# Optimization experiments

Hardware: AMD Instinct MI355X
Metric: run time of the kernel (lower is better)

## Reference

```python
import jax, jax.numpy as jnp
import numpy as np


def setup_inputs() -> dict:
    key = jax.random.key(0)
    k_in, k_idx, k_neg, k_w, k_b = jax.random.split(key, 5)
    N, C_in, C_out, K, L = 8, 128, 256, 7, 16384
    x = jax.random.normal(k_in, (N, C_in, L), dtype=jnp.float32)
    idx = jax.random.randint(k_idx, (K, L), 0, L, dtype=jnp.int64)
    drop = jax.random.uniform(k_neg, (K, L)) < 0.05
    idx = jnp.where(drop, -1, idx)
    stdv = 1.0 / np.sqrt(C_in * K)
    weight = jax.random.uniform(k_w, (C_out, C_in, K), dtype=jnp.float32, minval=-stdv, maxval=stdv)
    bias = jax.random.uniform(k_b, (C_out,), dtype=jnp.float32, minval=-stdv, maxval=stdv)
    return {"input": x, "indices": idx, "weight": weight, "bias": bias}


def reference(input, indices, weight, bias):
    # indices: (K, L); -1 means zero-padding (matches utils.prepare_mask)
    mask = (indices >= 0).astype(input.dtype)          # (K, L)
    safe_idx = jnp.where(indices >= 0, indices, 0)     # (K, L)
    # im2col gather: (N, C_in, K, L), masked where neighbor is absent
    col = input[..., safe_idx] * mask
    # weight (C_out, C_in, K) contracted against col -> (N, C_out, L), mirrors bmm
    out = jnp.einsum('nckl,ock->nol', col, weight)
    out = out + bias[None, :, None]
    return out
```

## Files before the change

kernel.cpp:

```cpp
#include <hip/hip_runtime.h>
#include <stdint.h>

#define NB 8
#define CI 128
#define CO 256
#define KS 7
#define LL 16384
#define CK (CI * KS)

typedef _Float16 half8 __attribute__((ext_vector_type(8)));
typedef _Float16 half2v __attribute__((ext_vector_type(2)));
typedef float floatx4 __attribute__((ext_vector_type(4)));

__device__ __forceinline__ void load16_to_lds(const void* g, void* l) {
    __builtin_amdgcn_global_load_lds(
        (const __attribute__((address_space(1))) void*)g,
        (__attribute__((address_space(3))) void*)l, 16, 0, 0);
}

__global__ __launch_bounds__(256) void convert_x(const float* __restrict__ x,
                                                 _Float16* __restrict__ xT) {
    __shared__ float tile[32][129];
    const int n  = blockIdx.z;
    const int c0 = blockIdx.y * 32;
    const int l0 = blockIdx.x * 128;
    const int t  = threadIdx.x;
    const float* xs = x + (size_t)n * CI * LL + (size_t)c0 * LL + l0;
    {
        const int lj = t & 127, ci = t >> 7;
        #pragma unroll
        for (int it = 0; it < 16; ++it)
            tile[ci + it * 2][lj] = xs[(size_t)(ci + it * 2) * LL + lj];
    }
    __syncthreads();
    _Float16* xd = xT + (size_t)n * LL * CI + (size_t)l0 * CI + c0;
    const int cp = t & 15, lr = t >> 4;
    #pragma unroll
    for (int it = 0; it < 8; ++it) {
        const int l = lr + it * 16;
        half2v v;
        v[0] = (_Float16)tile[cp * 2][l];
        v[1] = (_Float16)tile[cp * 2 + 1][l];
        *(half2v*)(xd + (size_t)l * CI + cp * 2) = v;
    }
}

__global__ __launch_bounds__(256) void convert_w(const float* __restrict__ w,
                                                 _Float16* __restrict__ wT) {
    const int t = blockIdx.x * 256 + threadIdx.x;
    if (t >= CO * CK) return;
    const int o = t / CK;
    const int r = t - o * CK;
    const int k = r >> 7;
    const int c = r & 127;
    wT[t] = (_Float16)w[(size_t)o * CK + c * KS + k];
}

__global__ void zero_fill(float* __restrict__ z) {
    z[threadIdx.x] = 0.f;
}

__global__ __launch_bounds__(256) void iconv_mfma(
    const _Float16* __restrict__ xT,
    const int*      __restrict__ idx,
    const _Float16* __restrict__ wT,
    const float*    __restrict__ bias,
    const _Float16* __restrict__ zrow,
    float*          __restrict__ out)
{
    __shared__ _Float16 a_lds[128 * 32];
    __shared__ _Float16 b_lds[128 * 32];

    const int l0 = blockIdx.x * 128;
    const int o0 = blockIdx.y * 128;
    const int n  = blockIdx.z;
    const int t  = threadIdx.x;
    const int lane = t & 63;
    const int wv = t >> 6;
    const int wo = (wv >> 1) * 64;
    const int wl = (wv & 1) * 64;
    const int m16 = lane & 15;
    const int q8  = (lane >> 4) * 8;

    floatx4 acc[4][4];
    #pragma unroll
    for (int i = 0; i < 4; ++i)
        #pragma unroll
        for (int j = 0; j < 4; ++j) acc[i][j] = (floatx4)0.f;

    const int row  = t >> 2;
    const int part = t & 3;
    const _Float16* wbase0 = wT + (size_t)(o0 + row) * CK + part * 8;
    const _Float16* wbase1 = wT + (size_t)(o0 + 64 + row) * CK + part * 8;
    const _Float16* xbase  = xT + (size_t)n * LL * CI;
    const _Float16* zbase  = zrow + part * 8;

    for (int k = 0; k < KS; ++k) {
        const int i0 = idx[k * LL + l0 + row];
        const int i1 = idx[k * LL + l0 + 64 + row];
        const _Float16* s0 = (i0 >= 0) ? xbase + (size_t)i0 * CI + part * 8 : zbase;
        const _Float16* s1 = (i1 >= 0) ? xbase + (size_t)i1 * CI + part * 8 : zbase;
        const _Float16* w0 = wbase0 + k * CI;
        const _Float16* w1 = wbase1 + k * CI;
        for (int c0 = 0; c0 < CI; c0 += 32) {
            __syncthreads();
            load16_to_lds(s0 + c0, b_lds + t * 8);
            load16_to_lds(s1 + c0, b_lds + (256 + t) * 8);
            load16_to_lds(w0 + c0, a_lds + t * 8);
            load16_to_lds(w1 + c0, a_lds + (256 + t) * 8);
            __syncthreads();

            half8 af[4], bf[4];
            #pragma unroll
            for (int mf = 0; mf < 4; ++mf)
                af[mf] = *(const half8*)(a_lds + (wo + mf * 16 + m16) * 32 + q8);
            #pragma unroll
            for (int nf = 0; nf < 4; ++nf)
                bf[nf] = *(const half8*)(b_lds + (wl + nf * 16 + m16) * 32 + q8);
            #pragma unroll
            for (int mf = 0; mf < 4; ++mf)
                #pragma unroll
                for (int nf = 0; nf < 4; ++nf)
                    acc[mf][nf] = __builtin_amdgcn_mfma_f32_16x16x32_f16(
                        af[mf], bf[nf], acc[mf][nf], 0, 0, 0);
        }
    }

    const int r4 = (lane >> 4) * 4;
    #pragma unroll
    for (int mf = 0; mf < 4; ++mf) {
        const int obase = o0 + wo + mf * 16 + r4;
        const floatx4 b4 = *(const floatx4*)(bias + obase);
        #pragma unroll
        for (int nf = 0; nf < 4; ++nf) {
            const int l = l0 + wl + nf * 16 + m16;
            float* op = out + ((size_t)n * CO + obase) * LL + l;
            #pragma unroll
            for (int r = 0; r < 4; ++r)
                op[(size_t)r * LL] = acc[mf][nf][r] + b4[r];
        }
    }
}

__global__ __launch_bounds__(256) void iconv_fallback(
    const float* __restrict__ x, const int* __restrict__ idx,
    const float* __restrict__ w, const float* __restrict__ bias,
    float* __restrict__ out)
{
    __shared__ float col[CI][64];
    const int n  = blockIdx.y;
    const int l0 = blockIdx.x * 64;
    const int t  = threadIdx.x;
    const int ot = t & 63, lt = t >> 6;
    const int j = t >> 2, part = t & 3;
    float acc[4][16];
    #pragma unroll
    for (int oo = 0; oo < 4; ++oo) {
        const float bv = bias[ot * 4 + oo];
        #pragma unroll
        for (int ll = 0; ll < 16; ++ll) acc[oo][ll] = bv;
    }
    for (int k = 0; k < KS; ++k) {
        __syncthreads();
        const int i = idx[k * LL + l0 + j];
        const float* xr = x + (size_t)n * CI * LL;
        for (int q = 0; q < 32; ++q) {
            const int c = part * 32 + q;
            col[c][j] = (i >= 0) ? xr[(size_t)c * LL + i] : 0.f;
        }
        __syncthreads();
        for (int c = 0; c < CI; ++c) {
            const float* bv = &col[c][lt * 16];
            float wv[4];
            #pragma unroll
            for (int oo = 0; oo < 4; ++oo)
                wv[oo] = w[(size_t)(ot * 4 + oo) * CK + c * KS + k];
            #pragma unroll
            for (int oo = 0; oo < 4; ++oo)
                #pragma unroll
                for (int ll = 0; ll < 16; ++ll)
                    acc[oo][ll] += wv[oo] * bv[ll];
        }
    }
    #pragma unroll
    for (int oo = 0; oo < 4; ++oo) {
        float* orow = out + ((size_t)n * CO + (ot * 4 + oo)) * LL + l0 + lt * 16;
        #pragma unroll
        for (int q = 0; q < 16; ++q) orow[q] = acc[oo][q];
    }
}

extern "C" void kernel_launch(void* const* d_in, const int* in_sizes, int n_in,
                              void* d_out, int out_size, void* d_ws, size_t ws_size,
                              hipStream_t stream) {
    const float* x    = (const float*)d_in[0];
    const int*   idx  = (const int*)d_in[1];
    const float* w    = (const float*)d_in[2];
    const float* bias = (const float*)d_in[3];
    float* out = (float*)d_out;

    const size_t xt_bytes = (size_t)NB * LL * CI * sizeof(_Float16);
    const size_t wt_bytes = (size_t)CO * CK * sizeof(_Float16);
    const size_t need = xt_bytes + wt_bytes + 256;

    if (ws_size >= need) {
        _Float16* xT = (_Float16*)d_ws;
        _Float16* wT = (_Float16*)((char*)d_ws + xt_bytes);
        float*    zr = (float*)((char*)d_ws + xt_bytes + wt_bytes);
        convert_x<<<dim3(LL / 128, CI / 32, NB), 256, 0, stream>>>(x, xT);
        convert_w<<<dim3((CO * CK + 255) / 256), 256, 0, stream>>>(w, wT);
        zero_fill<<<1, 64, 0, stream>>>(zr);
        iconv_mfma<<<dim3(LL / 128, CO / 128, NB), 256, 0, stream>>>(
            xT, idx, wT, bias, (const _Float16*)zr, out);
    } else {
        iconv_fallback<<<dim3(LL / 64, NB), 256, 0, stream>>>(x, idx, w, bias, out);
    }
}
```

Baseline: 263.6 us.

## Widen MFMA K-tile to 64, preload indices, vectorize x transpose, fold zero row

The main conv kernel now stages 64 channels per LDS tile instead of 32, which halves the number of barrier pairs and doubles the MFMA work done per sync. All seven index rows are preloaded into registers up front. The x conversion kernel is rewritten to use float4 loads, packed half2 LDS storage and 16-byte stores. The zero-fill kernel is removed by storing the padding zero row at the end of the converted weight buffer. The cost is twice the LDS use per block and more registers held for the indices, which could lower occupancy.

```diff
diff --git a/kernel.cpp b/kernel.cpp
--- a/kernel.cpp
+++ b/kernel.cpp
@@ -11,6 +11,7 @@
 typedef _Float16 half8 __attribute__((ext_vector_type(8)));
 typedef _Float16 half2v __attribute__((ext_vector_type(2)));
 typedef float floatx4 __attribute__((ext_vector_type(4)));
+typedef uint32_t uintx4 __attribute__((ext_vector_type(4)));
 
 __device__ __forceinline__ void load16_to_lds(const void* g, void* l) {
     __builtin_amdgcn_global_load_lds(
@@ -20,44 +21,56 @@
 
 __global__ __launch_bounds__(256) void convert_x(const float* __restrict__ x,
                                                  _Float16* __restrict__ xT) {
-    __shared__ float tile[32][129];
-    const int n  = blockIdx.z;
-    const int c0 = blockIdx.y * 32;
-    const int l0 = blockIdx.x * 128;
+    __shared__ uint32_t tile[64][65];
+    const int n  = blockIdx.y;
+    const int l0 = blockIdx.x * 64;
     const int t  = threadIdx.x;
-    const float* xs = x + (size_t)n * CI * LL + (size_t)c0 * LL + l0;
-    {
-        const int lj = t & 127, ci = t >> 7;
-        #pragma unroll
-        for (int it = 0; it < 16; ++it)
-            tile[ci + it * 2][lj] = xs[(size_t)(ci + it * 2) * LL + lj];
+    const float* xs = x + (size_t)n * CI * LL + l0;
+
+    const int l4  = (t & 15) * 4;
+    const int cpr = t >> 4;
+    #pragma unroll
+    for (int p = 0; p < 4; ++p) {
+        const int cp = cpr + p * 16;
+        const float4 a4 = *(const float4*)(xs + (size_t)(2 * cp) * LL + l4);
+        const float4 b4 = *(const float4*)(xs + (size_t)(2 * cp + 1) * LL + l4);
+        half2v h;
+        h[0] = (_Float16)a4.x; h[1] = (_Float16)b4.x;
+        tile[l4 + 0][cp] = __builtin_bit_cast(uint32_t, h);
+        h[0] = (_Float16)a4.y; h[1] = (_Float16)b4.y;
+        tile[l4 + 1][cp] = __builtin_bit_cast(uint32_t, h);
+        h[0] = (_Float16)a4.z; h[1] = (_Float16)b4.z;
+        tile[l4 + 2][cp] = __builtin_bit_cast(uint32_t, h);
+        h[0] = (_Float16)a4.w; h[1] = (_Float16)b4.w;
+        tile[l4 + 3][cp] = __builtin_bit_cast(uint32_t, h);
     }
     __syncthreads();
-    _Float16* xd = xT + (size_t)n * LL * CI + (size_t)l0 * CI + c0;
-    const int cp = t & 15, lr = t >> 4;
-    #pragma unroll
-    for (int it = 0; it < 8; ++it) {
-        const int l = lr + it * 16;
-        half2v v;
-        v[0] = (_Float16)tile[cp * 2][l];
-        v[1] = (_Float16)tile[cp * 2 + 1][l];
-        *(half2v*)(xd + (size_t)l * CI + cp * 2) = v;
+
+    const int lw  = t >> 4;
+    const int cp0 = (t & 15) * 4;
+    _Float16* xd = xT + (size_t)n * LL * CI + (size_t)l0 * CI;
+    #pragma unroll
+    for (int p = 0; p < 4; ++p) {
+        const int l = lw + p * 16;
+        uintx4 d;
+        d[0] = tile[l][cp0 + 0];
+        d[1] = tile[l][cp0 + 1];
+        d[2] = tile[l][cp0 + 2];
+        d[3] = tile[l][cp0 + 3];
+        *(uintx4*)(xd + (size_t)l * CI + cp0 * 2) = d;
     }
 }
 
 __global__ __launch_bounds__(256) void convert_w(const float* __restrict__ w,
                                                  _Float16* __restrict__ wT) {
     const int t = blockIdx.x * 256 + threadIdx.x;
-    if (t >= CO * CK) return;
+    if (t >= CO * CK + 128) return;
+    if (t >= CO * CK) { wT[t] = (_Float16)0.f; return; }
     const int o = t / CK;
     const int r = t - o * CK;
     const int k = r >> 7;
     const int c = r & 127;
     wT[t] = (_Float16)w[(size_t)o * CK + c * KS + k];
-}
-
-__global__ void zero_fill(float* __restrict__ z) {
-    z[threadIdx.x] = 0.f;
 }
 
 __global__ __launch_bounds__(256) void iconv_mfma(
@@ -68,8 +81,8 @@
     const _Float16* __restrict__ zrow,
     float*          __restrict__ out)
 {
-    __shared__ _Float16 a_lds[128 * 32];
-    __shared__ _Float16 b_lds[128 * 32];
+    __shared__ _Float16 a_lds[128 * 64];
+    __shared__ _Float16 b_lds[128 * 64];
 
     const int l0 = blockIdx.x * 128;
     const int o0 = blockIdx.y * 128;
@@ -88,41 +101,51 @@
         #pragma unroll
         for (int j = 0; j < 4; ++j) acc[i][j] = (floatx4)0.f;
 
-    const int row  = t >> 2;
-    const int part = t & 3;
-    const _Float16* wbase0 = wT + (size_t)(o0 + row) * CK + part * 8;
-    const _Float16* wbase1 = wT + (size_t)(o0 + 64 + row) * CK + part * 8;
-    const _Float16* xbase  = xT + (size_t)n * LL * CI;
-    const _Float16* zbase  = zrow + part * 8;
+    const int srow = t >> 3;
+    const int part = t & 7;
+
+    int iv[KS][4];
+    #pragma unroll
+    for (int k = 0; k < KS; ++k)
+        #pragma unroll
+        for (int i = 0; i < 4; ++i)
+            iv[k][i] = idx[k * LL + l0 + i * 32 + srow];
+
+    const _Float16* xbase = xT + (size_t)n * LL * CI;
+    const _Float16* wbase = wT + (size_t)(o0 + srow) * CK + part * 8;
+    const int dst = srow * 64 + part * 8;
 
     for (int k = 0; k < KS; ++k) {
-        const int i0 = idx[k * LL + l0 + row];
-        const int i1 = idx[k * LL + l0 + 64 + row];
-        const _Float16* s0 = (i0 >= 0) ? xbase + (size_t)i0 * CI + part * 8 : zbase;
-        const _Float16* s1 = (i1 >= 0) ? xbase + (size_t)i1 * CI + part * 8 : zbase;
-        const _Float16* w0 = wbase0 + k * CI;
-        const _Float16* w1 = wbase1 + k * CI;
-        for (int c0 = 0; c0 < CI; c0 += 32) {
+        for (int c0 = 0; c0 < CI; c0 += 64) {
             __syncthreads();
-            load16_to_lds(s0 + c0, b_lds + t * 8);
-            load16_to_lds(s1 + c0, b_lds + (256 + t) * 8);
-            load16_to_lds(w0 + c0, a_lds + t * 8);
-            load16_to_lds(w1 + c0, a_lds + (256 + t) * 8);
+            #pragma unroll
+            for (int i = 0; i < 4; ++i) {
+                const int ii = iv[k][i];
+                const _Float16* bs = (ii >= 0)
+                    ? (xbase + (size_t)ii * CI + c0 + part * 8)
+                    : (zrow + c0 + part * 8);
+                load16_to_lds(bs, b_lds + i * 2048 + dst);
+                load16_to_lds(wbase + (size_t)i * 32 * CK + k * CI + c0,
+                              a_lds + i * 2048 + dst);
+            }
             __syncthreads();
 
-            half8 af[4], bf[4];
-            #pragma unroll
-            for (int mf = 0; mf < 4; ++mf)
-                af[mf] = *(const half8*)(a_lds + (wo + mf * 16 + m16) * 32 + q8);
-            #pragma unroll
-            for (int nf = 0; nf < 4; ++nf)
-                bf[nf] = *(const half8*)(b_lds + (wl + nf * 16 + m16) * 32 + q8);
-            #pragma unroll
-            for (int mf = 0; mf < 4; ++mf)
+            #pragma unroll
+            for (int kk = 0; kk < 2; ++kk) {
+                half8 af[4], bf[4];
+                #pragma unroll
+                for (int mf = 0; mf < 4; ++mf)
+                    af[mf] = *(const half8*)(a_lds + (wo + mf * 16 + m16) * 64 + kk * 32 + q8);
                 #pragma unroll
                 for (int nf = 0; nf < 4; ++nf)
-                    acc[mf][nf] = __builtin_amdgcn_mfma_f32_16x16x32_f16(
-                        af[mf], bf[nf], acc[mf][nf], 0, 0, 0);
+                    bf[nf] = *(const half8*)(b_lds + (wl + nf * 16 + m16) * 64 + kk * 32 + q8);
+                #pragma unroll
+                for (int mf = 0; mf < 4; ++mf)
+                    #pragma unroll
+                    for (int nf = 0; nf < 4; ++nf)
+                        acc[mf][nf] = __builtin_amdgcn_mfma_f32_16x16x32_f16(
+                            af[mf], bf[nf], acc[mf][nf], 0, 0, 0);
+            }
         }
     }
 
@@ -200,18 +223,17 @@
     float* out = (float*)d_out;
 
     const size_t xt_bytes = (size_t)NB * LL * CI * sizeof(_Float16);
-    const size_t wt_bytes = (size_t)CO * CK * sizeof(_Float16);
-    const size_t need = xt_bytes + wt_bytes + 256;
+    const size_t wt_elems = (size_t)CO * CK + 128;
+    const size_t need = xt_bytes + wt_elems * sizeof(_Float16);
 
     if (ws_size >= need) {
         _Float16* xT = (_Float16*)d_ws;
         _Float16* wT = (_Float16*)((char*)d_ws + xt_bytes);
-        float*    zr = (float*)((char*)d_ws + xt_bytes + wt_bytes);
-        convert_x<<<dim3(LL / 128, CI / 32, NB), 256, 0, stream>>>(x, xT);
-        convert_w<<<dim3((CO * CK + 255) / 256), 256, 0, stream>>>(w, wT);
-        zero_fill<<<1, 64, 0, stream>>>(zr);
+        const _Float16* zr = wT + (size_t)CO * CK;
+        convert_x<<<dim3(LL / 64, NB), 256, 0, stream>>>(x, xT);
+        convert_w<<<dim3(((int)wt_elems + 255) / 256), 256, 0, stream>>>(w, wT);
         iconv_mfma<<<dim3(LL / 128, CO / 128, NB), 256, 0, stream>>>(
-            xT, idx, wT, bias, (const _Float16*)zr, out);
+            xT, idx, wT, bias, zr, out);
     } else {
         iconv_fallback<<<dim3(LL / 64, NB), 256, 0, stream>>>(x, idx, w, bias, out);
     }
```

Result: no change. 261.8 us (-0.7%).
